# Kernel optimization log

Hardware: AMD Instinct MI355X
Metric: run time of the kernel (lower is better)

Reference implementation:

```python
import jax, jax.numpy as jnp
import numpy as np

N = 4096      # total nodes (target + context)
T = 1024      # target nodes
C = N - T     # context nodes
F = 128       # raw node feature dim
H = 512       # num_hids
HEADS = 16    # num_heads
D = H // HEADS
WIN = 2       # window_size
L = 2         # num_layers
E_T = 65536   # edges: target queries -> context keys
E_C = 98304   # edges: context queries -> target keys
EDGE_ENC = 8
EDGE_DIST = 8
SCALE = D ** -0.5


def setup_inputs():
    key = jax.random.key(0)
    ks = iter(jax.random.split(key, 40))
    s = 0.02
    rn = lambda shp, sc=1.0: jax.random.normal(next(ks), shp, jnp.float32) * sc
    return {
        "node_feats": rn((N, F)),
        "edge_emb_table": rn((EDGE_ENC * WIN, H), s),
        "edge_dist_emb_table": rn((EDGE_DIST, H), s),
        "w_node": rn((F, H), s), "b_node": jnp.zeros((H,), jnp.float32),
        "w_edge_enc": rn((H, HEADS), s), "b_edge_enc": jnp.zeros((HEADS,), jnp.float32),
        "w_edge_dist": rn((H, HEADS), s), "b_edge_dist": jnp.zeros((HEADS,), jnp.float32),
        "ln1_g": jnp.ones((L, H), jnp.float32), "ln1_b": jnp.zeros((L, H), jnp.float32),
        "attn1_w": rn((L, 4, H, H), s), "attn1_b": jnp.zeros((L, 4, H), jnp.float32),
        "attn2_w": rn((L, 4, H, H), s), "attn2_b": jnp.zeros((L, 4, H), jnp.float32),
        "ln2_g": jnp.ones((L, H), jnp.float32), "ln2_b": jnp.zeros((L, H), jnp.float32),
        "ffn_w1": rn((L, H, H), s), "ffn_b1": jnp.zeros((L, H), jnp.float32),
        "ffn_w2": rn((L, H, H), s), "ffn_b2": jnp.zeros((L, H), jnp.float32),
        "edge_encodes": jax.random.randint(next(ks), (N, N, WIN), 0, EDGE_ENC * WIN, jnp.int32),
        "edge_dist_encodes": jax.random.randint(next(ks), (N, N), 0, EDGE_DIST, jnp.int32),
        "target_sparse_row": jax.random.randint(next(ks), (E_T,), 0, T, jnp.int32),
        "target_sparse_col": jax.random.randint(next(ks), (E_T,), 0, C, jnp.int32),
        "context_sparse_row": jax.random.randint(next(ks), (E_C,), 0, C, jnp.int32),
        "context_sparse_col": jax.random.randint(next(ks), (E_C,), 0, T, jnp.int32),
        "target_node_size": T,
    }


def _ln(x, g, b, eps=1e-5):
    m = jnp.mean(x, -1, keepdims=True)
    v = jnp.mean((x - m) ** 2, -1, keepdims=True)
    return (x - m) * jax.lax.rsqrt(v + eps) * g + b


def _seg_softmax(x, idx, n):
    # scatter-max / scatter-sum softmax over edges grouped by row index
    m = jax.ops.segment_max(x, idx, num_segments=n)
    m = jnp.where(jnp.isfinite(m), m, 0.0)  # empty segments
    e = jnp.exp(x - m[idx])
    s = jax.ops.segment_sum(e, idx, num_segments=n)
    return e / (s[idx] + 1e-16)


def _emb(table, idx):
    # nn.Embedding(max_norm=True): looked-up rows renormed to L2 norm <= 1
    e = table[idx]
    nrm = jnp.linalg.norm(e, axis=-1, keepdims=True)
    return e / jnp.maximum(nrm, 1.0)


def _mha(yq, ykv, w, b, bias, row, col, n_out):
    # w: [4,H,H] = q,k,v,o projections; b: [4,H]
    q = (yq @ w[0] + b[0]).reshape(-1, HEADS, D)
    k = (ykv @ w[1] + b[1]).reshape(-1, HEADS, D)
    v = (ykv @ w[2] + b[2]).reshape(-1, HEADS, D)
    s = jnp.einsum('ehd,ehd->eh', q[row], k[col]) * SCALE + bias  # [E,HEADS]
    a = _seg_softmax(s, row, n_out)
    o = jax.ops.segment_sum(a[:, :, None] * v[col], row, num_segments=n_out)
    return o.reshape(-1, H) @ w[3] + b[3]


def _forward(node_feats, edge_emb_table, edge_dist_emb_table, w_node, b_node,
             w_edge_enc, b_edge_enc, w_edge_dist, b_edge_dist,
             ln1_g, ln1_b, attn1_w, attn1_b, attn2_w, attn2_b,
             ln2_g, ln2_b, ffn_w1, ffn_b1, ffn_w2, ffn_b2,
             edge_encodes, edge_dist_encodes,
             target_sparse_row, target_sparse_col,
             context_sparse_row, context_sparse_col, Tn):
    Cn = node_feats.shape[0] - Tn

    def bias_for(rows, cols):
        # get_encodings: mean over window of edge embedding, plus dist embedding
        e1 = jnp.mean(_emb(edge_emb_table, edge_encodes[rows, cols]), axis=-2)  # [E,H]
        b1 = e1 @ w_edge_enc + b_edge_enc
        e2 = _emb(edge_dist_emb_table, edge_dist_encodes[rows, cols])           # [E,H]
        b2 = e2 @ w_edge_dist + b_edge_dist
        return b1 + b2                                                           # [E,HEADS]

    attn_bias_target = bias_for(target_sparse_row, target_sparse_col + Tn)
    attn_bias_context = bias_for(context_sparse_row + Tn, context_sparse_col)

    x = node_feats @ w_node + b_node
    for l in range(L):
        y = _ln(x, ln1_g[l], ln1_b[l])
        y_t, y_c = y[:Tn], y[Tn:]
        out1 = _mha(y_t, y_c, attn1_w[l], attn1_b[l], attn_bias_target,
                    target_sparse_row, target_sparse_col, Tn)    # [T,H]
        out2 = _mha(y_c, y_t, attn2_w[l], attn2_b[l], attn_bias_context,
                    context_sparse_row, context_sparse_col, Cn)  # [C,H]
        # original code: y_all = cat([y_target_, y_context_]) = [attn2 out, attn1 out]
        x = x + jnp.concatenate([out2, out1], axis=0)
        y = _ln(x, ln2_g[l], ln2_b[l])
        y = jax.nn.gelu(y @ ffn_w1[l] + ffn_b1[l], approximate=False) @ ffn_w2[l] + ffn_b2[l]
        x = x + y
    return x


def reference(node_feats, edge_emb_table, edge_dist_emb_table, w_node, b_node,
              w_edge_enc, b_edge_enc, w_edge_dist, b_edge_dist,
              ln1_g, ln1_b, attn1_w, attn1_b, attn2_w, attn2_b,
              ln2_g, ln2_b, ffn_w1, ffn_b1, ffn_w2, ffn_b2,
              edge_encodes, edge_dist_encodes,
              target_sparse_row, target_sparse_col,
              context_sparse_row, context_sparse_col, target_node_size):
    return _forward(node_feats, edge_emb_table, edge_dist_emb_table, w_node, b_node,
                    w_edge_enc, b_edge_enc, w_edge_dist, b_edge_dist,
                    ln1_g, ln1_b, attn1_w, attn1_b, attn2_w, attn2_b,
                    ln2_g, ln2_b, ffn_w1, ffn_b1, ffn_w2, ffn_b2,
                    edge_encodes, edge_dist_encodes,
                    target_sparse_row, target_sparse_col,
                    context_sparse_row, context_sparse_col, target_node_size)
```

## Files before the change

### kernel.cpp

```cpp
#include <hip/hip_runtime.h>
#include <math.h>

#define N_NODES 4096
#define T_NODES 1024
#define C_NODES 3072
#define F_IN    128
#define H_DIM   512
#define HEADS   16
#define D_HEAD  32
#define E_T     65536
#define E_C     98304
#define SCALE_QK 0.17677669529663687f

typedef __attribute__((ext_vector_type(8))) short short8;
typedef __attribute__((ext_vector_type(4))) float f32x4;
typedef __attribute__((ext_vector_type(2))) float f32x2;

struct ushort4_t { unsigned short x, y, z, w; };

__device__ inline unsigned short f2bf(float f) {
    unsigned u = __float_as_uint(f);
    unsigned r = (u + 0x7fffu + ((u >> 16) & 1u)) >> 16;
    return (unsigned short)r;
}
__device__ inline float bf2f(unsigned short u) {
    return __uint_as_float(((unsigned)u) << 16);
}

__device__ inline void gload16(const void* g, void* l) {
    __builtin_amdgcn_global_load_lds(
        (const __attribute__((address_space(1))) unsigned int*)g,
        (__attribute__((address_space(3))) unsigned int*)l, 16, 0, 0);
}

struct TD { const float* src[20]; unsigned short* dst[20]; };

__global__ void prep_kernel(TD d, const float* __restrict__ w_node, unsigned short* __restrict__ wnT,
                            const float* __restrict__ nf, unsigned short* __restrict__ nfb)
{
    int z = blockIdx.z;
    __shared__ float tile[32][33];
    int tr = threadIdx.x >> 5, tc = threadIdx.x & 31;
    if (z < 20) {
        const float* src = d.src[z];
        unsigned short* dst = d.dst[z];
        int r0 = blockIdx.y * 32, c0 = blockIdx.x * 32;
        #pragma unroll
        for (int p = 0; p < 4; ++p) tile[tr + 8*p][tc] = src[(size_t)(r0 + tr + 8*p)*512 + c0 + tc];
        __syncthreads();
        #pragma unroll
        for (int p = 0; p < 4; ++p) dst[(size_t)(c0 + tr + 8*p)*512 + r0 + tc] = f2bf(tile[tc][tr + 8*p]);
    } else if (z == 20) {
        if (blockIdx.y >= 4) return;
        int r0 = blockIdx.y * 32, c0 = blockIdx.x * 32;
        #pragma unroll
        for (int p = 0; p < 4; ++p) tile[tr + 8*p][tc] = w_node[(size_t)(r0 + tr + 8*p)*512 + c0 + tc];
        __syncthreads();
        #pragma unroll
        for (int p = 0; p < 4; ++p) wnT[(size_t)(c0 + tr + 8*p)*128 + r0 + tc] = f2bf(tile[tc][tr + 8*p]);
    } else {
        int gid = (blockIdx.y * 16 + blockIdx.x) * 256 + threadIdx.x;
        #pragma unroll
        for (int rep = 0; rep < 2; ++rep) {
            int i = gid + rep * 65536;
            float4 v = ((const float4*)nf)[i];
            ushort4_t o = { f2bf(v.x), f2bf(v.y), f2bf(v.z), f2bf(v.w) };
            ((ushort4_t*)nfb)[i] = o;
        }
    }
}

__global__ void proj_kernel(const float* __restrict__ emb, const float* __restrict__ dist_emb,
                            const float* __restrict__ w_enc, const float* __restrict__ w_dist,
                            const float* __restrict__ a1b, const float* __restrict__ a2b,
                            float* __restrict__ P1, float* __restrict__ P2,
                            float* __restrict__ bct, float* __restrict__ bcc)
{
    if (blockIdx.x == 96) {
        int t = threadIdx.x;
        for (int l = 0; l < 2; ++l)
            for (int i = t; i < 512; i += 256) {
                bct[l*1536 + i]        = a1b[(l*4+0)*512 + i];
                bct[l*1536 + 512 + i]  = a2b[(l*4+1)*512 + i];
                bct[l*1536 + 1024 + i] = a2b[(l*4+2)*512 + i];
                bcc[l*1536 + i]        = a1b[(l*4+1)*512 + i];
                bcc[l*1536 + 512 + i]  = a1b[(l*4+2)*512 + i];
                bcc[l*1536 + 1024 + i] = a2b[(l*4+0)*512 + i];
            }
        return;
    }
    int wid = threadIdx.x >> 6, lane = threadIdx.x & 63;
    int o = blockIdx.x * 4 + wid;
    const float* src; const float* wm; float* dst; int h;
    if (o < 256) { src = emb      + (size_t)(o >> 4) * 512; wm = w_enc;  h = o & 15;  dst = P1 + o; }
    else { int o2 = o - 256; src = dist_emb + (size_t)(o2 >> 4) * 512; wm = w_dist; h = o2 & 15; dst = P2 + o2; }
    float4 v0 = ((const float4*)src)[lane*2];
    float4 v1 = ((const float4*)src)[lane*2+1];
    float nrm = v0.x*v0.x + v0.y*v0.y + v0.z*v0.z + v0.w*v0.w
              + v1.x*v1.x + v1.y*v1.y + v1.z*v1.z + v1.w*v1.w;
    int f0 = lane * 8;
    float dt = v0.x*wm[(f0+0)*16+h] + v0.y*wm[(f0+1)*16+h] + v0.z*wm[(f0+2)*16+h] + v0.w*wm[(f0+3)*16+h]
             + v1.x*wm[(f0+4)*16+h] + v1.y*wm[(f0+5)*16+h] + v1.z*wm[(f0+6)*16+h] + v1.w*wm[(f0+7)*16+h];
    #pragma unroll
    for (int s = 1; s < 64; s <<= 1) { nrm += __shfl_xor(nrm, s, 64); dt += __shfl_xor(dt, s, 64); }
    if (lane == 0) *dst = dt / fmaxf(sqrtf(nrm), 1.0f);
}

__global__ void hist2_kernel(const int* __restrict__ t_row, const int* __restrict__ c_row,
                             int* __restrict__ cnt_t, int* __restrict__ cnt_c) {
    int i = blockIdx.x * 256 + threadIdx.x;
    if (i < E_T) atomicAdd(&cnt_t[t_row[i]], 1);
    else atomicAdd(&cnt_c[c_row[i - E_T]], 1);
}

__global__ void scan2_kernel(const int* __restrict__ cnt_t, int* __restrict__ off_t, int* __restrict__ cur_t,
                             const int* __restrict__ cnt_c, int* __restrict__ off_c, int* __restrict__ cur_c) {
    const int* counts; int* offsets; int* cursor; int n;
    if (blockIdx.x == 0) { counts = cnt_t; offsets = off_t; cursor = cur_t; n = T_NODES; }
    else                 { counts = cnt_c; offsets = off_c; cursor = cur_c; n = C_NODES; }
    __shared__ int lds[1024];
    int t = threadIdx.x;
    int c = (n + 1023) / 1024;
    int base = t * c;
    int s = 0;
    for (int j = 0; j < c; ++j) { int i = base + j; if (i < n) s += counts[i]; }
    lds[t] = s;
    __syncthreads();
    for (int d = 1; d < 1024; d <<= 1) {
        int v = (t >= d) ? lds[t-d] : 0;
        __syncthreads();
        lds[t] += v;
        __syncthreads();
    }
    int run = lds[t] - s;
    for (int j = 0; j < c; ++j) {
        int i = base + j;
        if (i < n) { offsets[i] = run; cursor[i] = run; run += counts[i]; }
    }
    if (t == 1023) offsets[n] = lds[1023];
}

__global__ void scatter2_kernel(const int* __restrict__ t_row, const int* __restrict__ c_row,
                                int* __restrict__ cur_t, int* __restrict__ cur_c,
                                int* __restrict__ perm_t, int* __restrict__ perm_c) {
    int i = blockIdx.x * 256 + threadIdx.x;
    if (i < E_T) { int p = atomicAdd(&cur_t[t_row[i]], 1); perm_t[p] = i; }
    else { int j = i - E_T; int p = atomicAdd(&cur_c[c_row[j]], 1); perm_c[p] = j; }
}

__global__ void bias2_kernel(const int* __restrict__ t_row, const int* __restrict__ t_col,
                             const int* __restrict__ c_row, const int* __restrict__ c_col,
                             const int* __restrict__ perm_t, const int* __restrict__ perm_c,
                             const int* __restrict__ enc, const int* __restrict__ dist,
                             const float* __restrict__ P1, const float* __restrict__ P2,
                             const float* __restrict__ b_enc, const float* __restrict__ b_dist,
                             float* __restrict__ biasp_t, float* __restrict__ biasp_c,
                             int* __restrict__ colp_t, int* __restrict__ colp_c)
{
    __shared__ float sP1[256], sP2[128], sb[16];
    int t = threadIdx.x;
    sP1[t] = P1[t];
    if (t < 128) sP2[t] = P2[t];
    if (t < 16)  sb[t]  = b_enc[t] + b_dist[t];
    __syncthreads();
    int gi = blockIdx.x * 256 + t;
    if (gi < E_T) {
        int i = gi; int e = perm_t[i];
        long r = t_row[e]; long c = t_col[e];
        long idx = r * N_NODES + c + T_NODES;
        int i1 = enc[idx*2], i2 = enc[idx*2+1], j = dist[idx];
        colp_t[i] = (int)c;
        #pragma unroll
        for (int h = 0; h < 16; ++h)
            biasp_t[(size_t)i*16 + h] = 0.5f*(sP1[i1*16+h] + sP1[i2*16+h]) + sP2[j*16+h] + sb[h];
    } else {
        int i = gi - E_T; int e = perm_c[i];
        long r = c_row[e] + T_NODES; long c = c_col[e];
        long idx = r * N_NODES + c;
        int i1 = enc[idx*2], i2 = enc[idx*2+1], j = dist[idx];
        colp_c[i] = (int)c;
        #pragma unroll
        for (int h = 0; h < 16; ++h)
            biasp_c[(size_t)i*16 + h] = 0.5f*(sP1[i1*16+h] + sP1[i2*16+h]) + sP2[j*16+h] + sb[h];
    }
}

__global__ void ln_kernel(const float* __restrict__ x, const float* __restrict__ g,
                          const float* __restrict__ b, unsigned short* __restrict__ y, int M) {
    int wave = threadIdx.x >> 6;
    int lane = threadIdx.x & 63;
    int row = blockIdx.x * 4 + wave;
    if (row >= M) return;
    const float4* xr = (const float4*)(x + (size_t)row * H_DIM);
    float4 a = xr[lane*2], c4 = xr[lane*2+1];
    float s  = a.x + a.y + a.z + a.w + c4.x + c4.y + c4.z + c4.w;
    float sq = a.x*a.x + a.y*a.y + a.z*a.z + a.w*a.w + c4.x*c4.x + c4.y*c4.y + c4.z*c4.z + c4.w*c4.w;
    #pragma unroll
    for (int o = 1; o < 64; o <<= 1) { s += __shfl_xor(s, o, 64); sq += __shfl_xor(sq, o, 64); }
    float mean = s * (1.0f/512.0f);
    float var  = sq * (1.0f/512.0f) - mean*mean;
    float inv  = rsqrtf(var + 1e-5f);
    const float4* gp = (const float4*)g;
    const float4* bp = (const float4*)b;
    float4 g0 = gp[lane*2], g1 = gp[lane*2+1];
    float4 b0 = bp[lane*2], b1 = bp[lane*2+1];
    ushort4_t o0 = { f2bf((a.x-mean)*inv*g0.x + b0.x), f2bf((a.y-mean)*inv*g0.y + b0.y),
                     f2bf((a.z-mean)*inv*g0.z + b0.z), f2bf((a.w-mean)*inv*g0.w + b0.w) };
    ushort4_t o1 = { f2bf((c4.x-mean)*inv*g1.x + b1.x), f2bf((c4.y-mean)*inv*g1.y + b1.y),
                     f2bf((c4.z-mean)*inv*g1.z + b1.z), f2bf((c4.w-mean)*inv*g1.w + b1.w) };
    ushort4_t* yr = (ushort4_t*)(y + (size_t)row * H_DIM);
    yr[lane*2] = o0; yr[lane*2+1] = o1;
}

template <int MODE>
__global__ __launch_bounds__(256) void gemm_bf16(
    const unsigned short* __restrict__ A, int lda,
    const unsigned short* __restrict__ Wa, const unsigned short* __restrict__ Wb, int ldb,
    const float* __restrict__ biasa, const float* __restrict__ biasb,
    void* __restrict__ Cout, int ldc, int K, int mswitch)
{
    __shared__ unsigned short As[2][128*32];
    __shared__ unsigned short Bs[2][64*32];
    int tid  = threadIdx.x;
    int wid  = tid >> 6, lane = tid & 63;
    int wm   = wid >> 1, wn = wid & 1;
    int m0   = blockIdx.y * 128, n0 = blockIdx.x * 64;
    const unsigned short* BT = (m0 >= mswitch) ? Wb : Wa;
    const float* bias        = (m0 >= mswitch) ? biasb : biasa;

    int srow  = lane >> 2;
    int sslot = lane & 3;
    const unsigned short* Ag0 = A  + (size_t)(m0 + wid*32 + srow)*lda + sslot*8;
    const unsigned short* Ag1 = Ag0 + (size_t)16*lda;
    const unsigned short* Bg0 = BT + (size_t)(n0 + wid*16 + srow)*ldb + sslot*8;

    f32x4 acc[4][2] = {};
    int NT = K >> 5;

    auto stage = [&](int bsel, int kt) {
        char* abase = (char*)&As[bsel][0] + wid*2048;
        char* bbase = (char*)&Bs[bsel][0] + wid*1024;
        gload16(Ag0 + kt*32, abase);
        gload16(Ag1 + kt*32, abase + 1024);
        gload16(Bg0 + kt*32, bbase);
    };

    stage(0, 0);
    __syncthreads();
    int cur = 0;
    int arowf = wm*64 + (lane & 15);
    int kslot = (lane >> 4) * 8;
    for (int kt = 0; kt < NT; ++kt) {
        if (kt + 1 < NT) stage(cur ^ 1, kt + 1);
        const unsigned short* as = &As[cur][0];
        const unsigned short* bs = &Bs[cur][0];
        short8 af[4], bf[2];
        #pragma unroll
        for (int fm = 0; fm < 4; ++fm)
            af[fm] = *(const short8*)&as[(arowf + fm*16)*32 + kslot];
        #pragma unroll
        for (int fn = 0; fn < 2; ++fn)
            bf[fn] = *(const short8*)&bs[(wn*32 + fn*16 + (lane & 15))*32 + kslot];
        #pragma unroll
        for (int fm = 0; fm < 4; ++fm)
            #pragma unroll
            for (int fn = 0; fn < 2; ++fn)
                acc[fm][fn] = __builtin_amdgcn_mfma_f32_16x16x32_bf16(af[fm], bf[fn], acc[fm][fn], 0, 0, 0);
        __syncthreads();
        cur ^= 1;
    }

    int crow = m0 + wm*64 + (lane >> 4)*4;
    int ccol = n0 + wn*32 + (lane & 15);
    #pragma unroll
    for (int fn = 0; fn < 2; ++fn) {
        float bv = bias[ccol + fn*16];
        #pragma unroll
        for (int fm = 0; fm < 4; ++fm) {
            #pragma unroll
            for (int j = 0; j < 4; ++j) {
                float val = acc[fm][fn][j] + bv;
                size_t off = (size_t)(crow + fm*16 + j)*ldc + ccol + fn*16;
                if (MODE == 0) {
                    ((float*)Cout)[off] = val;
                } else if (MODE == 1) {
                    float gl = 0.5f * val * (1.0f + erff(val * 0.70710678118654752f));
                    ((unsigned short*)Cout)[off] = f2bf(gl);
                } else if (MODE == 2) {
                    ((float*)Cout)[off] += val;
                } else {
                    ((unsigned short*)Cout)[off] = f2bf(val);
                }
            }
        }
    }
}

__global__ void cvt_kv8_kernel(const unsigned short* __restrict__ qkv, unsigned char* __restrict__ kv8)
{
    int gid = blockIdx.x * 256 + threadIdx.x;
    int row = gid >> 7;
    int ch  = gid & 127;
    int colbase = (row < T_NODES) ? 512 : 0;
    short8 s = *(const short8*)(qkv + (size_t)row*1536 + colbase + ch*8);
    float f[8];
    #pragma unroll
    for (int j = 0; j < 8; ++j) f[j] = bf2f((unsigned short)s[j]);
    int lo = 0, hi = 0;
    lo = __builtin_amdgcn_cvt_pk_fp8_f32(f[0], f[1], lo, false);
    lo = __builtin_amdgcn_cvt_pk_fp8_f32(f[2], f[3], lo, true);
    hi = __builtin_amdgcn_cvt_pk_fp8_f32(f[4], f[5], hi, false);
    hi = __builtin_amdgcn_cvt_pk_fp8_f32(f[6], f[7], hi, true);
    int2 o = { lo, hi };
    *(int2*)(kv8 + (size_t)row*1024 + ch*8) = o;
}

__global__ __launch_bounds__(256) void attn_fused(
    const unsigned short* __restrict__ qkv,
    const unsigned char* __restrict__ kv8,
    const float* __restrict__ biasp_t, const float* __restrict__ biasp_c,
    const int* __restrict__ off_t, const int* __restrict__ colp_t,
    const int* __restrict__ off_c, const int* __restrict__ colp_c,
    unsigned short* __restrict__ ob)
{
    __shared__ float mrg[2][64][9];
    int wave = threadIdx.x >> 6, lane = threadIdx.x & 63;
    int rowslot = wave >> 1;
    int half    = wave & 1;
    int g = blockIdx.x * 2 + rowslot;

    int r, orow, rowbase;
    size_t qoff;
    const float* biasE; const int* offs; const int* colp;
    if (g < T_NODES) {
        r = g;
        qoff = (size_t)r * 1536;
        rowbase = T_NODES;
        biasE = biasp_t; offs = off_t; colp = colp_t;
        orow = C_NODES + r;
    } else {
        r = g - T_NODES;
        qoff = (size_t)(T_NODES + r) * 1536 + 1024;
        rowbase = 0;
        biasE = biasp_c; offs = off_c; colp = colp_c;
        orow = r;
    }

    float qf[8];
    {
        short8 qq = *(const short8*)(qkv + qoff + lane*8);
        #pragma unroll
        for (int j = 0; j < 8; ++j) qf[j] = bf2f((unsigned short)qq[j]);
    }
    int h4 = lane >> 2;

    int beg = offs[r], end = offs[r+1];
    float lsum = 0.f;
    float acc[8];
    #pragma unroll
    for (int j = 0; j < 8; ++j) acc[j] = 0.f;

    for (int i0 = beg + half*4; i0 < end; i0 += 8) {
        bool okk[4]; int cc[4]; float bb[4];
        uint2 kk[4], vv[4];
        #pragma unroll
        for (int u = 0; u < 4; ++u) {
            int ii = i0 + u;
            okk[u] = ii < end;
            cc[u]  = okk[u] ? colp[ii] : 0;
            bb[u]  = okk[u] ? biasE[(size_t)ii*16 + h4] : 0.f;
            const unsigned char* base = kv8 + (size_t)(rowbase + cc[u])*1024 + lane*8;
            kk[u] = *(const uint2*)base;
            vv[u] = *(const uint2*)(base + 512);
        }
        #pragma unroll
        for (int u = 0; u < 4; ++u) {
            f32x2 ka = __builtin_amdgcn_cvt_pk_f32_fp8(kk[u].x, false);
            f32x2 kb = __builtin_amdgcn_cvt_pk_f32_fp8(kk[u].x, true);
            f32x2 kc = __builtin_amdgcn_cvt_pk_f32_fp8(kk[u].y, false);
            f32x2 kd = __builtin_amdgcn_cvt_pk_f32_fp8(kk[u].y, true);
            float d = qf[0]*ka.x + qf[1]*ka.y + qf[2]*kb.x + qf[3]*kb.y
                    + qf[4]*kc.x + qf[5]*kc.y + qf[6]*kd.x + qf[7]*kd.y;
            d += __shfl_xor(d, 1, 64);
            d += __shfl_xor(d, 2, 64);
            float s = d * SCALE_QK + bb[u];
            float pw = okk[u] ? __expf(s) : 0.f;
            lsum += pw;
            f32x2 va = __builtin_amdgcn_cvt_pk_f32_fp8(vv[u].x, false);
            f32x2 vb = __builtin_amdgcn_cvt_pk_f32_fp8(vv[u].x, true);
            f32x2 vc = __builtin_amdgcn_cvt_pk_f32_fp8(vv[u].y, false);
            f32x2 vd = __builtin_amdgcn_cvt_pk_f32_fp8(vv[u].y, true);
            acc[0] += pw * va.x; acc[1] += pw * va.y;
            acc[2] += pw * vb.x; acc[3] += pw * vb.y;
            acc[4] += pw * vc.x; acc[5] += pw * vc.y;
            acc[6] += pw * vd.x; acc[7] += pw * vd.y;
        }
    }

    if (half == 1) {
        #pragma unroll
        for (int j = 0; j < 8; ++j) mrg[rowslot][lane][j] = acc[j];
        mrg[rowslot][lane][8] = lsum;
    }
    __syncthreads();
    if (half == 0) {
        #pragma unroll
        for (int j = 0; j < 8; ++j) acc[j] += mrg[rowslot][lane][j];
        lsum += mrg[rowslot][lane][8];
        float inv = 1.0f / (lsum + 1e-16f);
        ushort4_t o0 = { f2bf(acc[0]*inv), f2bf(acc[1]*inv), f2bf(acc[2]*inv), f2bf(acc[3]*inv) };
        ushort4_t o1 = { f2bf(acc[4]*inv), f2bf(acc[5]*inv), f2bf(acc[6]*inv), f2bf(acc[7]*inv) };
        ushort4_t* op = (ushort4_t*)(ob + (size_t)orow * H_DIM + lane*8);
        op[0] = o0; op[1] = o1;
    }
}

extern "C" void kernel_launch(void* const* d_in, const int* in_sizes, int n_in,
                              void* d_out, int out_size, void* d_ws, size_t ws_size,
                              hipStream_t stream)
{
    const float* node_feats = (const float*)d_in[0];
    const float* edge_emb   = (const float*)d_in[1];
    const float* dist_emb   = (const float*)d_in[2];
    const float* w_node     = (const float*)d_in[3];
    const float* b_node     = (const float*)d_in[4];
    const float* w_enc      = (const float*)d_in[5];
    const float* b_enc      = (const float*)d_in[6];
    const float* w_dist     = (const float*)d_in[7];
    const float* b_dist     = (const float*)d_in[8];
    const float* ln1_g      = (const float*)d_in[9];
    const float* ln1_b      = (const float*)d_in[10];
    const float* attn1_w    = (const float*)d_in[11];
    const float* attn1_b    = (const float*)d_in[12];
    const float* attn2_w    = (const float*)d_in[13];
    const float* attn2_b    = (const float*)d_in[14];
    const float* ln2_g      = (const float*)d_in[15];
    const float* ln2_b      = (const float*)d_in[16];
    const float* ffn_w1     = (const float*)d_in[17];
    const float* ffn_b1     = (const float*)d_in[18];
    const float* ffn_w2     = (const float*)d_in[19];
    const float* ffn_b2     = (const float*)d_in[20];
    const int* enc          = (const int*)d_in[21];
    const int* dist         = (const int*)d_in[22];
    const int* t_row        = (const int*)d_in[23];
    const int* t_col        = (const int*)d_in[24];
    const int* c_row        = (const int*)d_in[25];
    const int* c_col        = (const int*)d_in[26];

    float* x = (float*)d_out;

    char* w = (char*)d_ws;
    auto alloc = [&](size_t bytes) { char* p = w; w += (bytes + 255) & ~(size_t)255; return p; };

    unsigned short* qkv  = (unsigned short*)alloc((size_t)N_NODES*1536*2);
    unsigned short* nfb  = qkv;
    unsigned short* h1   = qkv;
    unsigned char* kv8   = (unsigned char*)alloc((size_t)N_NODES*1024);
    unsigned short* yb   = (unsigned short*)alloc((size_t)N_NODES*H_DIM*2);
    unsigned short* ob   = (unsigned short*)alloc((size_t)N_NODES*H_DIM*2);
    float* biasp_t       = (float*)alloc((size_t)E_T*HEADS*4);
    float* biasp_c       = (float*)alloc((size_t)E_C*HEADS*4);
    int* colp_t          = (int*)alloc((size_t)E_T*4);
    int* colp_c          = (int*)alloc((size_t)E_C*4);
    int* cnt_t           = (int*)alloc(T_NODES*4);
    int* cnt_c           = (int*)alloc(C_NODES*4);
    int* off_t           = (int*)alloc((T_NODES+1)*4);
    int* cur_t           = (int*)alloc(T_NODES*4);
    int* perm_t          = (int*)alloc((size_t)E_T*4);
    int* off_c           = (int*)alloc((C_NODES+1)*4);
    int* cur_c           = (int*)alloc(C_NODES*4);
    int* perm_c          = (int*)alloc((size_t)E_C*4);
    float* P1            = (float*)alloc(256*4);
    float* P2            = (float*)alloc(128*4);
    unsigned short* wcat_t = (unsigned short*)alloc((size_t)2*1536*512*2);
    unsigned short* wcat_c = (unsigned short*)alloc((size_t)2*1536*512*2);
    unsigned short* wo1    = (unsigned short*)alloc((size_t)2*512*512*2);
    unsigned short* wo2    = (unsigned short*)alloc((size_t)2*512*512*2);
    unsigned short* wf1    = (unsigned short*)alloc((size_t)2*512*512*2);
    unsigned short* wf2    = (unsigned short*)alloc((size_t)2*512*512*2);
    unsigned short* wnT    = (unsigned short*)alloc((size_t)H_DIM*F_IN*2);
    float* bcat_t        = (float*)alloc(2*1536*4);
    float* bcat_c        = (float*)alloc(2*1536*4);

    const size_t SZ = 512*512;
    const int BIG = 1 << 30;

    TD td;
    for (int l = 0; l < 2; ++l) {
        int b = l*10;
        td.src[b+0] = attn1_w + (size_t)(l*4+0)*SZ;  td.dst[b+0] = wcat_t + (size_t)l*1536*512;
        td.src[b+1] = attn2_w + (size_t)(l*4+1)*SZ;  td.dst[b+1] = wcat_t + (size_t)l*1536*512 + SZ;
        td.src[b+2] = attn2_w + (size_t)(l*4+2)*SZ;  td.dst[b+2] = wcat_t + (size_t)l*1536*512 + 2*SZ;
        td.src[b+3] = attn1_w + (size_t)(l*4+1)*SZ;  td.dst[b+3] = wcat_c + (size_t)l*1536*512;
        td.src[b+4] = attn1_w + (size_t)(l*4+2)*SZ;  td.dst[b+4] = wcat_c + (size_t)l*1536*512 + SZ;
        td.src[b+5] = attn2_w + (size_t)(l*4+0)*SZ;  td.dst[b+5] = wcat_c + (size_t)l*1536*512 + 2*SZ;
        td.src[b+6] = attn1_w + (size_t)(l*4+3)*SZ;  td.dst[b+6] = wo1 + (size_t)l*SZ;
        td.src[b+7] = attn2_w + (size_t)(l*4+3)*SZ;  td.dst[b+7] = wo2 + (size_t)l*SZ;
        td.src[b+8] = ffn_w1  + (size_t)l*SZ;        td.dst[b+8] = wf1 + (size_t)l*SZ;
        td.src[b+9] = ffn_w2  + (size_t)l*SZ;        td.dst[b+9] = wf2 + (size_t)l*SZ;
    }
    prep_kernel<<<dim3(16,16,22), 256, 0, stream>>>(td, w_node, wnT, node_feats, nfb);
    proj_kernel<<<97, 256, 0, stream>>>(edge_emb, dist_emb, w_enc, w_dist,
                                        attn1_b, attn2_b, P1, P2, bcat_t, bcat_c);

    hipMemsetAsync(cnt_t, 0, (T_NODES + C_NODES)*4, stream);
    hist2_kernel<<<(E_T+E_C)/256, 256, 0, stream>>>(t_row, c_row, cnt_t, cnt_c);
    scan2_kernel<<<2, 1024, 0, stream>>>(cnt_t, off_t, cur_t, cnt_c, off_c, cur_c);
    scatter2_kernel<<<(E_T+E_C)/256, 256, 0, stream>>>(t_row, c_row, cur_t, cur_c, perm_t, perm_c);
    bias2_kernel<<<(E_T+E_C)/256, 256, 0, stream>>>(t_row, t_col, c_row, c_col, perm_t, perm_c,
                                                    enc, dist, P1, P2, b_enc, b_dist,
                                                    biasp_t, biasp_c, colp_t, colp_c);

    gemm_bf16<0><<<dim3(8, 32), 256, 0, stream>>>(nfb, F_IN, wnT, wnT, F_IN,
                                                  b_node, b_node, x, H_DIM, F_IN, BIG);

    for (int l = 0; l < 2; ++l) {
        ln_kernel<<<N_NODES/4, 256, 0, stream>>>(x, ln1_g + l*H_DIM, ln1_b + l*H_DIM, yb, N_NODES);

        gemm_bf16<3><<<dim3(24, 32), 256, 0, stream>>>(yb, H_DIM,
            wcat_t + (size_t)l*1536*512, wcat_c + (size_t)l*1536*512, H_DIM,
            bcat_t + l*1536, bcat_c + l*1536, qkv, 1536, H_DIM, T_NODES);

        cvt_kv8_kernel<<<2048, 256, 0, stream>>>(qkv, kv8);

        attn_fused<<<N_NODES/2, 256, 0, stream>>>(
            qkv, kv8, biasp_t, biasp_c, off_t, colp_t, off_c, colp_c, ob);

        gemm_bf16<2><<<dim3(8, 32), 256, 0, stream>>>(ob, H_DIM,
            wo2 + (size_t)l*SZ, wo1 + (size_t)l*SZ, H_DIM,
            attn2_b + (size_t)(l*4+3)*H_DIM, attn1_b + (size_t)(l*4+3)*H_DIM,
            x, H_DIM, H_DIM, C_NODES);

        ln_kernel<<<N_NODES/4, 256, 0, stream>>>(x, ln2_g + l*H_DIM, ln2_b + l*H_DIM, yb, N_NODES);
        gemm_bf16<1><<<dim3(8, 32), 256, 0, stream>>>(yb, H_DIM,
            wf1 + (size_t)l*SZ, wf1 + (size_t)l*SZ, H_DIM,
            ffn_b1 + l*H_DIM, ffn_b1 + l*H_DIM, h1, H_DIM, H_DIM, BIG);
        gemm_bf16<2><<<dim3(8, 32), 256, 0, stream>>>(h1, H_DIM,
            wf2 + (size_t)l*SZ, wf2 + (size_t)l*SZ, H_DIM,
            ffn_b2 + l*H_DIM, ffn_b2 + l*H_DIM, x, H_DIM, H_DIM, BIG);
    }
}
```

Before: 268.9 us.

## Split each attention row across four waves and prefetch next edge indices

The attention kernel now assigns one destination row per block and splits its edge list across four waves instead of two, merging the partial sums through shared memory. It also software-prefetches the next iteration's column indices and bias values while the current K/V loads are in flight. This aims to raise memory-level parallelism on the irregular gather and shorten each row's serial edge loop. The cost is twice as many blocks, a larger cross-wave reduction, and extra registers for the prefetched values.

Result: faster. 262.6 us (-2.3%).

```diff
diff --git a/kernel.cpp b/kernel.cpp
--- a/kernel.cpp
+++ b/kernel.cpp
@@ -323,11 +323,9 @@
     const int* __restrict__ off_c, const int* __restrict__ colp_c,
     unsigned short* __restrict__ ob)
 {
-    __shared__ float mrg[2][64][9];
+    __shared__ float mrg[3][64][9];
     int wave = threadIdx.x >> 6, lane = threadIdx.x & 63;
-    int rowslot = wave >> 1;
-    int half    = wave & 1;
-    int g = blockIdx.x * 2 + rowslot;
+    int g = blockIdx.x;
 
     int r, orow, rowbase;
     size_t qoff;
@@ -360,19 +358,37 @@
     #pragma unroll
     for (int j = 0; j < 8; ++j) acc[j] = 0.f;
 
-    for (int i0 = beg + half*4; i0 < end; i0 += 8) {
-        bool okk[4]; int cc[4]; float bb[4];
+    int i0 = beg + wave*4;
+    int cc[4]; float bb[4]; bool okk[4];
+    #pragma unroll
+    for (int u = 0; u < 4; ++u) {
+        int ii = i0 + u;
+        okk[u] = ii < end;
+        cc[u]  = okk[u] ? colp[ii] : 0;
+        bb[u]  = okk[u] ? biasE[(size_t)ii*16 + h4] : 0.f;
+    }
+
+    for (; i0 < end; i0 += 16) {
+        int ccur[4]; float bcur[4]; bool ocur[4];
+        #pragma unroll
+        for (int u = 0; u < 4; ++u) { ccur[u] = cc[u]; bcur[u] = bb[u]; ocur[u] = okk[u]; }
+
         uint2 kk[4], vv[4];
         #pragma unroll
         for (int u = 0; u < 4; ++u) {
-            int ii = i0 + u;
+            const unsigned char* base = kv8 + (size_t)(rowbase + ccur[u])*1024 + lane*8;
+            kk[u] = *(const uint2*)base;
+            vv[u] = *(const uint2*)(base + 512);
+        }
+
+        #pragma unroll
+        for (int u = 0; u < 4; ++u) {
+            int ii = i0 + 16 + u;
             okk[u] = ii < end;
             cc[u]  = okk[u] ? colp[ii] : 0;
             bb[u]  = okk[u] ? biasE[(size_t)ii*16 + h4] : 0.f;
-            const unsigned char* base = kv8 + (size_t)(rowbase + cc[u])*1024 + lane*8;
-            kk[u] = *(const uint2*)base;
-            vv[u] = *(const uint2*)(base + 512);
         }
+
         #pragma unroll
         for (int u = 0; u < 4; ++u) {
             f32x2 ka = __builtin_amdgcn_cvt_pk_f32_fp8(kk[u].x, false);
@@ -383,8 +399,8 @@
                     + qf[4]*kc.x + qf[5]*kc.y + qf[6]*kd.x + qf[7]*kd.y;
             d += __shfl_xor(d, 1, 64);
             d += __shfl_xor(d, 2, 64);
-            float s = d * SCALE_QK + bb[u];
-            float pw = okk[u] ? __expf(s) : 0.f;
+            float s = d * SCALE_QK + bcur[u];
+            float pw = ocur[u] ? __expf(s) : 0.f;
             lsum += pw;
             f32x2 va = __builtin_amdgcn_cvt_pk_f32_fp8(vv[u].x, false);
             f32x2 vb = __builtin_amdgcn_cvt_pk_f32_fp8(vv[u].x, true);
@@ -397,16 +413,19 @@
         }
     }
 
-    if (half == 1) {
-        #pragma unroll
-        for (int j = 0; j < 8; ++j) mrg[rowslot][lane][j] = acc[j];
-        mrg[rowslot][lane][8] = lsum;
+    if (wave != 0) {
+        #pragma unroll
+        for (int j = 0; j < 8; ++j) mrg[wave-1][lane][j] = acc[j];
+        mrg[wave-1][lane][8] = lsum;
     }
     __syncthreads();
-    if (half == 0) {
-        #pragma unroll
-        for (int j = 0; j < 8; ++j) acc[j] += mrg[rowslot][lane][j];
-        lsum += mrg[rowslot][lane][8];
+    if (wave == 0) {
+        #pragma unroll
+        for (int w2 = 0; w2 < 3; ++w2) {
+            #pragma unroll
+            for (int j = 0; j < 8; ++j) acc[j] += mrg[w2][lane][j];
+            lsum += mrg[w2][lane][8];
+        }
         float inv = 1.0f / (lsum + 1e-16f);
         ushort4_t o0 = { f2bf(acc[0]*inv), f2bf(acc[1]*inv), f2bf(acc[2]*inv), f2bf(acc[3]*inv) };
         ushort4_t o1 = { f2bf(acc[4]*inv), f2bf(acc[5]*inv), f2bf(acc[6]*inv), f2bf(acc[7]*inv) };
@@ -523,7 +542,7 @@
 
         cvt_kv8_kernel<<<2048, 256, 0, stream>>>(qkv, kv8);
 
-        attn_fused<<<N_NODES/2, 256, 0, stream>>>(
+        attn_fused<<<N_NODES, 256, 0, stream>>>(
             qkv, kv8, biasp_t, biasp_c, off_t, colp_t, off_c, colp_c, ob);
 
         gemm_bf16<2><<<dim3(8, 32), 256, 0, stream>>>(ob, H_DIM,
```
